# Performance work log

Measured on AMD Instinct MI355X. Metric: run time of the kernel, lower is better.

The kernel has to match this reference:

```python
import jax, jax.numpy as jnp
import numpy as np

EMBED_DIM = 1024


def setup_inputs() -> dict:
    key = jax.random.key(0)
    ks = jax.random.split(key, 8)
    B, S, D = 4, 2048, EMBED_DIM
    scale = 1.0 / np.sqrt(D)
    x = jax.random.normal(ks[0], (B, S, D), dtype=jnp.float32)
    mask = jnp.zeros((S, S), dtype=jnp.float32)
    # nn.Linear default init ~ U(-1/sqrt(fan_in), 1/sqrt(fan_in)); exact dist irrelevant for correctness
    w_q = jax.random.uniform(ks[1], (D, D), jnp.float32, -scale, scale)
    b_q = jax.random.uniform(ks[2], (D,), jnp.float32, -scale, scale)
    w_k = jax.random.uniform(ks[3], (D, D), jnp.float32, -scale, scale)
    b_k = jax.random.uniform(ks[4], (D,), jnp.float32, -scale, scale)
    w_v = jax.random.uniform(ks[5], (D, D), jnp.float32, -scale, scale)
    b_v = jax.random.uniform(ks[6], (D,), jnp.float32, -scale, scale)
    return {"x": x, "mask": mask, "w_q": w_q, "b_q": b_q,
            "w_k": w_k, "b_k": b_k, "w_v": w_v, "b_v": b_v}


def reference(x, mask, w_q, b_q, w_k, b_k, w_v, b_v):
    D = x.shape[-1]
    # nn.Linear computes x @ W^T + b
    Q = jnp.einsum('bsd,ed->bse', x, w_q) + b_q
    K = jnp.einsum('bsd,ed->bse', x, w_k) + b_k
    V = jnp.einsum('bsd,ed->bse', x, w_v) + b_v
    scores = jnp.einsum('bqd,bkd->bqk', Q, K) / jnp.sqrt(jnp.asarray(D, x.dtype))
    scores = scores + mask  # additive mask, broadcast over batch
    attn = jax.nn.softmax(scores, axis=-1)
    return jnp.einsum('bqk,bkd->bqd', attn, V)
```

## Files before the change

kernel.cpp:

```cpp
#include <hip/hip_runtime.h>


typedef __attribute__((ext_vector_type(8))) short short8;
typedef __attribute__((ext_vector_type(4))) short short4v;
typedef __attribute__((ext_vector_type(4))) float float4v;

__device__ __forceinline__ short f2bf(float f) {
  unsigned u = __builtin_bit_cast(unsigned, f);
  u += 0x7fffu + ((u >> 16) & 1u);
  return (short)(u >> 16);
}
__device__ __forceinline__ float bf2f(short s) {
  unsigned u = ((unsigned)(unsigned short)s) << 16;
  return __builtin_bit_cast(float, u);
}

__device__ __forceinline__ void gl2lds16(const void* g, void* l) {
  __builtin_amdgcn_global_load_lds((const __attribute__((address_space(1))) void*)g,
                                   (__attribute__((address_space(3))) void*)l, 16, 0, 0);
}

__global__ __launch_bounds__(256) void prep_kernel(const float* __restrict__ x,
                                                   const float* __restrict__ wq,
                                                   const float* __restrict__ wk,
                                                   const float* __restrict__ wv,
                                                   const float* __restrict__ bq,
                                                   const float* __restrict__ bk,
                                                   short* __restrict__ x_bf,
                                                   short* __restrict__ w_bf,
                                                   float* __restrict__ bcat) {
  int b = blockIdx.x;
  if (b < 3072) {
    int seg = b >> 10;
    const float* w = seg == 0 ? wq : (seg == 1 ? wk : wv);
    int i = (b - (seg << 10)) * 256 + threadIdx.x;
    float4v v = ((const float4v*)w)[i];
    short4v o;
    o.x = f2bf(v.x); o.y = f2bf(v.y); o.z = f2bf(v.z); o.w = f2bf(v.w);
    ((short4v*)(w_bf + (long)seg * 1048576))[i] = o;
  } else if (b < 11264) {
    int i = (b - 3072) * 256 + threadIdx.x;
    float4v v = ((const float4v*)x)[i];
    short4v o;
    o.x = f2bf(v.x); o.y = f2bf(v.y); o.z = f2bf(v.z); o.w = f2bf(v.w);
    ((short4v*)x_bf)[i] = o;
  } else {
    int i = (b - 11264) * 256 + threadIdx.x;
    if (i < 2048) bcat[i] = i < 1024 ? bq[i] : bk[i - 1024];
  }
}

__device__ __forceinline__ void stage_half(const short* __restrict__ g, int ld,
                                           int grow0, int kt, short* lds, int t) {
  const int r = t >> 3;
  const int cch = (t & 7) ^ (r & 7);
  const long co = (long)kt + cch * 8;
  gl2lds16(g + (long)(grow0 + r) * ld + co, lds + t * 8);
  gl2lds16(g + (long)(grow0 + 64 + r) * ld + co, lds + 4096 + t * 8);
}

template <int EPI, int MH>
__device__ __forceinline__ void gemm_body(const short* __restrict__ A,
                                          const short* __restrict__ Bm,
                                          void* __restrict__ C,
                                          const float* __restrict__ aux,
                                          float* __restrict__ rsum, float scale,
                                          int N, int Kd, int Bld, int m0, int n0,
                                          short (*As)[64], short (*Bs)[64]) {
  const int t = threadIdx.x;
  const int lane = t & 63;
  const int wave = t >> 6;
  const int wm = (wave >> 2) * 64 * MH;
  const int wn = (wave & 3) * 64;
  const int col = lane & 15, quad = lane >> 4;
  const int sw = col & 7;
  const int NT = Kd >> 6;
  constexpr int AS = 128 * MH;

  float4v acc[4 * MH][4] = {};

  stage_half(A, Kd, m0, 0, &As[0][0], t);
  if constexpr (MH == 2) stage_half(A, Kd, m0 + 128, 0, &As[128][0], t);
  stage_half(Bm, Bld, n0, 0, &Bs[0][0], t);
  stage_half(Bm, Bld, n0 + 128, 0, &Bs[128][0], t);
  if (NT > 1) {
    stage_half(A, Kd, m0, 64, &As[AS][0], t);
    if constexpr (MH == 2) stage_half(A, Kd, m0 + 128, 64, &As[AS + 128][0], t);
    stage_half(Bm, Bld, n0, 64, &Bs[256][0], t);
    stage_half(Bm, Bld, n0 + 128, 64, &Bs[384][0], t);
    if constexpr (MH == 2)
      asm volatile("s_waitcnt vmcnt(8)" ::: "memory");
    else
      asm volatile("s_waitcnt vmcnt(6)" ::: "memory");
  } else {
    asm volatile("s_waitcnt vmcnt(0)" ::: "memory");
  }
  __builtin_amdgcn_s_barrier();

  int ar = 0;
  int aw = 2 * AS;
  int br = 0;

  for (int k = 0; k < NT; ++k) {
    short8 a[4][2], b0[2][2], b1[2][2];

    if constexpr (MH == 2) {
#pragma unroll
      for (int i = 0; i < 4; ++i)
#pragma unroll
        for (int s = 0; s < 2; ++s)
          a[i][s] = *(const short8*)&As[ar + wm + i * 16 + col][(((s * 4 + quad) ^ sw)) * 8];
#pragma unroll
      for (int j = 0; j < 2; ++j)
#pragma unroll
        for (int s = 0; s < 2; ++s)
          b0[j][s] = *(const short8*)&Bs[br + wn + j * 16 + col][(((s * 4 + quad) ^ sw)) * 8];
      if (k + 2 < NT) stage_half(A, Kd, m0, (k + 2) * 64, &As[aw][0], t);
      __builtin_amdgcn_s_barrier();
      __builtin_amdgcn_s_setprio(1);
#pragma unroll
      for (int i = 0; i < 4; ++i)
#pragma unroll
        for (int j = 0; j < 2; ++j)
#pragma unroll
          for (int s = 0; s < 2; ++s)
            acc[i][j] = __builtin_amdgcn_mfma_f32_16x16x32_bf16(a[i][s], b0[j][s], acc[i][j], 0, 0, 0);
      __builtin_amdgcn_s_setprio(0);

#pragma unroll
      for (int j = 0; j < 2; ++j)
#pragma unroll
        for (int s = 0; s < 2; ++s)
          b1[j][s] = *(const short8*)&Bs[br + wn + (j + 2) * 16 + col][(((s * 4 + quad) ^ sw)) * 8];
      if (k + 2 < NT) stage_half(A, Kd, m0 + 128, (k + 2) * 64, &As[aw + 128][0], t);
      __builtin_amdgcn_s_barrier();
      __builtin_amdgcn_s_setprio(1);
#pragma unroll
      for (int i = 0; i < 4; ++i)
#pragma unroll
        for (int j = 0; j < 2; ++j)
#pragma unroll
          for (int s = 0; s < 2; ++s)
            acc[i][j + 2] = __builtin_amdgcn_mfma_f32_16x16x32_bf16(a[i][s], b1[j][s], acc[i][j + 2], 0, 0, 0);
      __builtin_amdgcn_s_setprio(0);

#pragma unroll
      for (int i = 0; i < 4; ++i)
#pragma unroll
        for (int s = 0; s < 2; ++s)
          a[i][s] = *(const short8*)&As[ar + wm + (i + 4) * 16 + col][(((s * 4 + quad) ^ sw)) * 8];
      if (k + 2 < NT) stage_half(Bm, Bld, n0, (k + 2) * 64, &Bs[br][0], t);
      __builtin_amdgcn_s_barrier();
      __builtin_amdgcn_s_setprio(1);
#pragma unroll
      for (int i = 0; i < 4; ++i)
#pragma unroll
        for (int j = 0; j < 2; ++j)
#pragma unroll
          for (int s = 0; s < 2; ++s)
            acc[i + 4][j + 2] = __builtin_amdgcn_mfma_f32_16x16x32_bf16(a[i][s], b1[j][s], acc[i + 4][j + 2], 0, 0, 0);
      __builtin_amdgcn_s_setprio(0);

      if (k + 2 < NT) stage_half(Bm, Bld, n0 + 128, (k + 2) * 64, &Bs[br + 128][0], t);
      if (k + 2 < NT) {
        asm volatile("s_waitcnt vmcnt(8)" ::: "memory");
      } else if (k + 1 < NT) {
        asm volatile("s_waitcnt vmcnt(0)" ::: "memory");
      }
      __builtin_amdgcn_s_barrier();
      __builtin_amdgcn_s_setprio(1);
#pragma unroll
      for (int i = 0; i < 4; ++i)
#pragma unroll
        for (int j = 0; j < 2; ++j)
#pragma unroll
          for (int s = 0; s < 2; ++s)
            acc[i + 4][j] = __builtin_amdgcn_mfma_f32_16x16x32_bf16(a[i][s], b0[j][s], acc[i + 4][j], 0, 0, 0);
      __builtin_amdgcn_s_setprio(0);
    } else {
#pragma unroll
      for (int i = 0; i < 4; ++i)
#pragma unroll
        for (int s = 0; s < 2; ++s)
          a[i][s] = *(const short8*)&As[ar + wm + i * 16 + col][(((s * 4 + quad) ^ sw)) * 8];
#pragma unroll
      for (int j = 0; j < 2; ++j)
#pragma unroll
        for (int s = 0; s < 2; ++s)
          b0[j][s] = *(const short8*)&Bs[br + wn + j * 16 + col][(((s * 4 + quad) ^ sw)) * 8];
      if (k + 2 < NT) stage_half(A, Kd, m0, (k + 2) * 64, &As[aw][0], t);
      __builtin_amdgcn_s_barrier();
      __builtin_amdgcn_s_setprio(1);
#pragma unroll
      for (int i = 0; i < 4; ++i)
#pragma unroll
        for (int j = 0; j < 2; ++j)
#pragma unroll
          for (int s = 0; s < 2; ++s)
            acc[i][j] = __builtin_amdgcn_mfma_f32_16x16x32_bf16(a[i][s], b0[j][s], acc[i][j], 0, 0, 0);
      __builtin_amdgcn_s_setprio(0);

#pragma unroll
      for (int j = 0; j < 2; ++j)
#pragma unroll
        for (int s = 0; s < 2; ++s)
          b1[j][s] = *(const short8*)&Bs[br + wn + (j + 2) * 16 + col][(((s * 4 + quad) ^ sw)) * 8];
      if (k + 2 < NT) {
        stage_half(Bm, Bld, n0, (k + 2) * 64, &Bs[br][0], t);
        stage_half(Bm, Bld, n0 + 128, (k + 2) * 64, &Bs[br + 128][0], t);
        asm volatile("s_waitcnt vmcnt(6)" ::: "memory");
      } else if (k + 1 < NT) {
        asm volatile("s_waitcnt vmcnt(0)" ::: "memory");
      }
      __builtin_amdgcn_s_barrier();
      __builtin_amdgcn_s_setprio(1);
#pragma unroll
      for (int i = 0; i < 4; ++i)
#pragma unroll
        for (int j = 0; j < 2; ++j)
#pragma unroll
          for (int s = 0; s < 2; ++s)
            acc[i][j + 2] = __builtin_amdgcn_mfma_f32_16x16x32_bf16(a[i][s], b1[j][s], acc[i][j + 2], 0, 0, 0);
      __builtin_amdgcn_s_setprio(0);
    }

    ar = (ar == 2 * AS) ? 0 : ar + AS;
    aw = (aw == 2 * AS) ? 0 : aw + AS;
    br ^= 256;
  }

  float* invb = (float*)&Bs[0][0];
  if (EPI == 2) {
    __syncthreads();
    if (t < 128 * MH) {
      float s = 0.f;
#pragma unroll
      for (int p = 0; p < 32; ++p) s += aux[p * 8192 + m0 + t];
      invb[t] = __builtin_amdgcn_rcpf(s);
    }
    __syncthreads();
  }

  const float LOG2E = 1.44269504f;
  const float c1 = scale * LOG2E;
#pragma unroll
  for (int i = 0; i < 4 * MH; ++i) {
    float invv[4], addm[4], rsum4[4] = {0.f, 0.f, 0.f, 0.f};
    if (EPI == 2) {
#pragma unroll
      for (int r = 0; r < 4; ++r) invv[r] = invb[wm + i * 16 + quad * 4 + r];
    }
    if (EPI == 3) {
#pragma unroll
      for (int r = 0; r < 4; ++r) addm[r] = aux[m0 + wm + i * 16 + quad * 4 + r];
    }
#pragma unroll
    for (int j = 0; j < 4; ++j) {
      const int n = n0 + wn + j * 16 + col;
      float addn = 0.f;
      if (EPI == 0) addn = aux[n];
#pragma unroll
      for (int r = 0; r < 4; ++r) {
        const int m = m0 + wm + i * 16 + quad * 4 + r;
        float v = acc[i][j][r];
        if (EPI == 0) {
          ((short*)C)[(long)m * N + n] = f2bf(v + addn);
        } else if (EPI == 1) {
          float mv = aux[(long)m * N + n];
          float e = exp2f(fmaf(v, c1, mv * LOG2E));
          short q = f2bf(e);
          ((short*)C)[(long)m * N + n] = q;
          rsum4[r] += bf2f(q);
        } else if (EPI == 2) {
          ((float*)C)[(long)m * N + n] = v * invv[r];
        } else {
          ((short*)C)[(long)m * N + n] = f2bf(v + addm[r]);
        }
      }
    }
    if (EPI == 1) {
#pragma unroll
      for (int r = 0; r < 4; ++r) {
        float s = rsum4[r];
        s += __shfl_xor(s, 1);
        s += __shfl_xor(s, 2);
        s += __shfl_xor(s, 4);
        s += __shfl_xor(s, 8);
        if (col == 0)
          rsum[(wave & 3) * 8192 + m0 + wm + i * 16 + quad * 4 + r] = s;
      }
    }
  }
}

__global__ __launch_bounds__(512, 2) void qkv_kernel(const short* __restrict__ x_bf,
                                                     const short* __restrict__ w_bf,
                                                     short* __restrict__ QK,
                                                     short* __restrict__ Vt,
                                                     const float* __restrict__ bcat,
                                                     const float* __restrict__ bv) {
  __shared__ alignas(16) short As[768][64];
  __shared__ alignas(16) short Bs[512][64];
  const int b = blockIdx.x;
  const int g = (b & 7) * 48 + (b >> 3);
  if (g < 256) {
    const int pair = g >> 1, bz = g & 1;
    const int m0 = (pair >> 2) * 256, n0 = (pair & 3) * 256;
    gemm_body<0, 2>(x_bf, w_bf + (long)bz * 1048576, QK + (long)bz * 8388608,
                    bcat + bz * 1024, nullptr, 1.f, 1024, 1024, 1024, m0, n0, As, Bs);
  } else {
    const int v = g - 256;
    const int m0 = (v >> 5) * 256, n0 = (v & 31) * 256;
    gemm_body<3, 2>(w_bf + 2097152, x_bf, Vt, bv, nullptr, 1.f,
                    8192, 1024, 1024, m0, n0, As, Bs);
  }
}

__global__ __launch_bounds__(512, 2) void scores_kernel(const short* __restrict__ Q,
                                                        const short* __restrict__ Kb,
                                                        short* __restrict__ P,
                                                        const float* __restrict__ mask,
                                                        float* __restrict__ rspart) {
  __shared__ alignas(16) short As[768][64];
  __shared__ alignas(16) short Bs[512][64];
  const int b = blockIdx.x;
  const int g = (b & 7) * 32 + (b >> 3);
  const int bz = g >> 6, t2 = g & 63;
  const int m0 = (t2 >> 3) * 256, n0 = (t2 & 7) * 256;
  gemm_body<1, 2>(Q + (long)bz * 2097152, Kb + (long)bz * 2097152,
                  P + (long)bz * 4194304, mask,
                  rspart + (long)(n0 >> 8) * 4 * 8192 + bz * 2048, 0.03125f,
                  2048, 1024, 1024, m0, n0, As, Bs);
}

__global__ __launch_bounds__(512, 2) void pv_kernel(const short* __restrict__ P,
                                                    const short* __restrict__ Vt,
                                                    float* __restrict__ out,
                                                    const float* __restrict__ rspart) {
  __shared__ alignas(16) short As[384][64];
  __shared__ alignas(16) short Bs[512][64];
  const int b = blockIdx.x;
  const int g = (b & 7) * 32 + (b >> 3);
  const int bz = g >> 6, t2 = g & 63;
  const int m0 = (t2 >> 2) * 128, n0 = (t2 & 3) * 256;
  gemm_body<2, 1>(P + (long)bz * 4194304, Vt + (long)bz * 2048,
                  out + (long)bz * 2097152, rspart + bz * 2048, nullptr, 1.f,
                  1024, 2048, 8192, m0, n0, As, Bs);
}

extern "C" void kernel_launch(void* const* d_in, const int* in_sizes, int n_in,
                              void* d_out, int out_size, void* d_ws, size_t ws_size,
                              hipStream_t stream) {
  const float* x    = (const float*)d_in[0];
  const float* mask = (const float*)d_in[1];
  const float* wq   = (const float*)d_in[2];
  const float* bq   = (const float*)d_in[3];
  const float* wk   = (const float*)d_in[4];
  const float* bk   = (const float*)d_in[5];
  const float* wv   = (const float*)d_in[6];
  const float* bv   = (const float*)d_in[7];
  float* out = (float*)d_out;

  char* ws = (char*)d_ws;
  const size_t MB = 1024 * 1024;
  short* x_bf   = (short*)(ws);
  float* rspart = (float*)(ws);
  short* w_bf   = (short*)(ws + 16 * MB);
  short* QK     = (short*)(ws + 22 * MB);
  short* Vt     = (short*)(ws + 54 * MB);
  short* P      = (short*)(ws + 70 * MB);
  float* bcat   = (float*)(ws + 70 * MB);

  prep_kernel<<<11272, 256, 0, stream>>>(x, wq, wk, wv, bq, bk, x_bf, w_bf, bcat);

  qkv_kernel<<<384, 512, 0, stream>>>(x_bf, w_bf, QK, Vt, bcat, bv);

  short* Q  = QK;
  short* Kb = QK + 8388608;

  scores_kernel<<<256, 512, 0, stream>>>(Q, Kb, P, mask, rspart);

  pv_kernel<<<256, 512, 0, stream>>>(P, Vt, out, rspart);
}
```

Before: 255.4 us.

## Fuse prep, QKV, scores and PV into one cooperative persistent kernel

```diff
diff --git a/kernel.cpp b/kernel.cpp
--- a/kernel.cpp
+++ b/kernel.cpp
@@ -1,4 +1,7 @@
 #include <hip/hip_runtime.h>
+#include <hip/hip_cooperative_groups.h>
+
+namespace cg = cooperative_groups;
 
 
 typedef __attribute__((ext_vector_type(8))) short short8;
@@ -18,6 +21,335 @@
 __device__ __forceinline__ void gl2lds16(const void* g, void* l) {
   __builtin_amdgcn_global_load_lds((const __attribute__((address_space(1))) void*)g,
                                    (__attribute__((address_space(3))) void*)l, 16, 0, 0);
+}
+
+__device__ unsigned g_vt_ctr;
+
+__device__ __forceinline__ void stage_half(const short* __restrict__ g, int ld,
+                                           int grow0, int kt, short* lds, int t) {
+  const int r = t >> 3;
+  const int cch = (t & 7) ^ (r & 7);
+  const long co = (long)kt + cch * 8;
+  gl2lds16(g + (long)(grow0 + r) * ld + co, lds + t * 8);
+  gl2lds16(g + (long)(grow0 + 64 + r) * ld + co, lds + 4096 + t * 8);
+}
+
+template <int EPI, int MH>
+__device__ __forceinline__ void gemm_body(const short* __restrict__ A,
+                                          const short* __restrict__ Bm,
+                                          void* __restrict__ C,
+                                          const float* __restrict__ aux,
+                                          float* __restrict__ rsum, float scale,
+                                          int N, int Kd, int Bld, int m0, int n0,
+                                          short (*As)[64], short (*Bs)[64]) {
+  const int t = threadIdx.x;
+  const int lane = t & 63;
+  const int wave = t >> 6;
+  const int wm = (wave >> 2) * 64 * MH;
+  const int wn = (wave & 3) * 64;
+  const int col = lane & 15, quad = lane >> 4;
+  const int sw = col & 7;
+  const int NT = Kd >> 6;
+  constexpr int AS = 128 * MH;
+
+  float4v acc[4 * MH][4] = {};
+
+  stage_half(A, Kd, m0, 0, &As[0][0], t);
+  if constexpr (MH == 2) stage_half(A, Kd, m0 + 128, 0, &As[128][0], t);
+  stage_half(Bm, Bld, n0, 0, &Bs[0][0], t);
+  stage_half(Bm, Bld, n0 + 128, 0, &Bs[128][0], t);
+  if (NT > 1) {
+    stage_half(A, Kd, m0, 64, &As[AS][0], t);
+    if constexpr (MH == 2) stage_half(A, Kd, m0 + 128, 64, &As[AS + 128][0], t);
+    stage_half(Bm, Bld, n0, 64, &Bs[256][0], t);
+    stage_half(Bm, Bld, n0 + 128, 64, &Bs[384][0], t);
+    if constexpr (MH == 2)
+      asm volatile("s_waitcnt vmcnt(8)" ::: "memory");
+    else
+      asm volatile("s_waitcnt vmcnt(6)" ::: "memory");
+  } else {
+    asm volatile("s_waitcnt vmcnt(0)" ::: "memory");
+  }
+  __builtin_amdgcn_s_barrier();
+
+  int ar = 0;
+  int aw = 2 * AS;
+  int br = 0;
+
+  for (int k = 0; k < NT; ++k) {
+    short8 a[4][2], b0[2][2], b1[2][2];
+
+    if constexpr (MH == 2) {
+#pragma unroll
+      for (int i = 0; i < 4; ++i)
+#pragma unroll
+        for (int s = 0; s < 2; ++s)
+          a[i][s] = *(const short8*)&As[ar + wm + i * 16 + col][(((s * 4 + quad) ^ sw)) * 8];
+#pragma unroll
+      for (int j = 0; j < 2; ++j)
+#pragma unroll
+        for (int s = 0; s < 2; ++s)
+          b0[j][s] = *(const short8*)&Bs[br + wn + j * 16 + col][(((s * 4 + quad) ^ sw)) * 8];
+      if (k + 2 < NT) stage_half(A, Kd, m0, (k + 2) * 64, &As[aw][0], t);
+      __builtin_amdgcn_s_barrier();
+      __builtin_amdgcn_s_setprio(1);
+#pragma unroll
+      for (int i = 0; i < 4; ++i)
+#pragma unroll
+        for (int j = 0; j < 2; ++j)
+#pragma unroll
+          for (int s = 0; s < 2; ++s)
+            acc[i][j] = __builtin_amdgcn_mfma_f32_16x16x32_bf16(a[i][s], b0[j][s], acc[i][j], 0, 0, 0);
+      __builtin_amdgcn_s_setprio(0);
+
+#pragma unroll
+      for (int j = 0; j < 2; ++j)
+#pragma unroll
+        for (int s = 0; s < 2; ++s)
+          b1[j][s] = *(const short8*)&Bs[br + wn + (j + 2) * 16 + col][(((s * 4 + quad) ^ sw)) * 8];
+      if (k + 2 < NT) stage_half(A, Kd, m0 + 128, (k + 2) * 64, &As[aw + 128][0], t);
+      __builtin_amdgcn_s_barrier();
+      __builtin_amdgcn_s_setprio(1);
+#pragma unroll
+      for (int i = 0; i < 4; ++i)
+#pragma unroll
+        for (int j = 0; j < 2; ++j)
+#pragma unroll
+          for (int s = 0; s < 2; ++s)
+            acc[i][j + 2] = __builtin_amdgcn_mfma_f32_16x16x32_bf16(a[i][s], b1[j][s], acc[i][j + 2], 0, 0, 0);
+      __builtin_amdgcn_s_setprio(0);
+
+#pragma unroll
+      for (int i = 0; i < 4; ++i)
+#pragma unroll
+        for (int s = 0; s < 2; ++s)
+          a[i][s] = *(const short8*)&As[ar + wm + (i + 4) * 16 + col][(((s * 4 + quad) ^ sw)) * 8];
+      if (k + 2 < NT) stage_half(Bm, Bld, n0, (k + 2) * 64, &Bs[br][0], t);
+      __builtin_amdgcn_s_barrier();
+      __builtin_amdgcn_s_setprio(1);
+#pragma unroll
+      for (int i = 0; i < 4; ++i)
+#pragma unroll
+        for (int j = 0; j < 2; ++j)
+#pragma unroll
+          for (int s = 0; s < 2; ++s)
+            acc[i + 4][j + 2] = __builtin_amdgcn_mfma_f32_16x16x32_bf16(a[i][s], b1[j][s], acc[i + 4][j + 2], 0, 0, 0);
+      __builtin_amdgcn_s_setprio(0);
+
+      if (k + 2 < NT) stage_half(Bm, Bld, n0 + 128, (k + 2) * 64, &Bs[br + 128][0], t);
+      if (k + 2 < NT) {
+        asm volatile("s_waitcnt vmcnt(8)" ::: "memory");
+      } else if (k + 1 < NT) {
+        asm volatile("s_waitcnt vmcnt(0)" ::: "memory");
+      }
+      __builtin_amdgcn_s_barrier();
+      __builtin_amdgcn_s_setprio(1);
+#pragma unroll
+      for (int i = 0; i < 4; ++i)
+#pragma unroll
+        for (int j = 0; j < 2; ++j)
+#pragma unroll
+          for (int s = 0; s < 2; ++s)
+            acc[i + 4][j] = __builtin_amdgcn_mfma_f32_16x16x32_bf16(a[i][s], b0[j][s], acc[i + 4][j], 0, 0, 0);
+      __builtin_amdgcn_s_setprio(0);
+    } else {
+#pragma unroll
+      for (int i = 0; i < 4; ++i)
+#pragma unroll
+        for (int s = 0; s < 2; ++s)
+          a[i][s] = *(const short8*)&As[ar + wm + i * 16 + col][(((s * 4 + quad) ^ sw)) * 8];
+#pragma unroll
+      for (int j = 0; j < 2; ++j)
+#pragma unroll
+        for (int s = 0; s < 2; ++s)
+          b0[j][s] = *(const short8*)&Bs[br + wn + j * 16 + col][(((s * 4 + quad) ^ sw)) * 8];
+      if (k + 2 < NT) stage_half(A, Kd, m0, (k + 2) * 64, &As[aw][0], t);
+      __builtin_amdgcn_s_barrier();
+      __builtin_amdgcn_s_setprio(1);
+#pragma unroll
+      for (int i = 0; i < 4; ++i)
+#pragma unroll
+        for (int j = 0; j < 2; ++j)
+#pragma unroll
+          for (int s = 0; s < 2; ++s)
+            acc[i][j] = __builtin_amdgcn_mfma_f32_16x16x32_bf16(a[i][s], b0[j][s], acc[i][j], 0, 0, 0);
+      __builtin_amdgcn_s_setprio(0);
+
+#pragma unroll
+      for (int j = 0; j < 2; ++j)
+#pragma unroll
+        for (int s = 0; s < 2; ++s)
+          b1[j][s] = *(const short8*)&Bs[br + wn + (j + 2) * 16 + col][(((s * 4 + quad) ^ sw)) * 8];
+      if (k + 2 < NT) {
+        stage_half(Bm, Bld, n0, (k + 2) * 64, &Bs[br][0], t);
+        stage_half(Bm, Bld, n0 + 128, (k + 2) * 64, &Bs[br + 128][0], t);
+        asm volatile("s_waitcnt vmcnt(6)" ::: "memory");
+      } else if (k + 1 < NT) {
+        asm volatile("s_waitcnt vmcnt(0)" ::: "memory");
+      }
+      __builtin_amdgcn_s_barrier();
+      __builtin_amdgcn_s_setprio(1);
+#pragma unroll
+      for (int i = 0; i < 4; ++i)
+#pragma unroll
+        for (int j = 0; j < 2; ++j)
+#pragma unroll
+          for (int s = 0; s < 2; ++s)
+            acc[i][j + 2] = __builtin_amdgcn_mfma_f32_16x16x32_bf16(a[i][s], b1[j][s], acc[i][j + 2], 0, 0, 0);
+      __builtin_amdgcn_s_setprio(0);
+    }
+
+    ar = (ar == 2 * AS) ? 0 : ar + AS;
+    aw = (aw == 2 * AS) ? 0 : aw + AS;
+    br ^= 256;
+  }
+
+  float* invb = (float*)&Bs[0][0];
+  if (EPI == 2) {
+    __syncthreads();
+    if (t < 128 * MH) {
+      float s = 0.f;
+#pragma unroll
+      for (int p = 0; p < 32; ++p) s += aux[p * 8192 + m0 + t];
+      invb[t] = __builtin_amdgcn_rcpf(s);
+    }
+    __syncthreads();
+  }
+
+  const float LOG2E = 1.44269504f;
+  const float c1 = scale * LOG2E;
+#pragma unroll
+  for (int i = 0; i < 4 * MH; ++i) {
+    float invv[4], addm[4], rsum4[4] = {0.f, 0.f, 0.f, 0.f};
+    if (EPI == 2) {
+#pragma unroll
+      for (int r = 0; r < 4; ++r) invv[r] = invb[wm + i * 16 + quad * 4 + r];
+    }
+    if (EPI == 3) {
+#pragma unroll
+      for (int r = 0; r < 4; ++r) addm[r] = aux[m0 + wm + i * 16 + quad * 4 + r];
+    }
+#pragma unroll
+    for (int j = 0; j < 4; ++j) {
+      const int n = n0 + wn + j * 16 + col;
+      float addn = 0.f;
+      if (EPI == 0) addn = aux[n];
+#pragma unroll
+      for (int r = 0; r < 4; ++r) {
+        const int m = m0 + wm + i * 16 + quad * 4 + r;
+        float v = acc[i][j][r];
+        if (EPI == 0) {
+          ((short*)C)[(long)m * N + n] = f2bf(v + addn);
+        } else if (EPI == 1) {
+          float mv = aux[(long)m * N + n];
+          float e = exp2f(fmaf(v, c1, mv * LOG2E));
+          short q = f2bf(e);
+          ((short*)C)[(long)m * N + n] = q;
+          rsum4[r] += bf2f(q);
+        } else if (EPI == 2) {
+          ((float*)C)[(long)m * N + n] = v * invv[r];
+        } else {
+          ((short*)C)[(long)m * N + n] = f2bf(v + addm[r]);
+        }
+      }
+    }
+    if (EPI == 1) {
+#pragma unroll
+      for (int r = 0; r < 4; ++r) {
+        float s = rsum4[r];
+        s += __shfl_xor(s, 1);
+        s += __shfl_xor(s, 2);
+        s += __shfl_xor(s, 4);
+        s += __shfl_xor(s, 8);
+        if (col == 0)
+          rsum[(wave & 3) * 8192 + m0 + wm + i * 16 + quad * 4 + r] = s;
+      }
+    }
+  }
+}
+
+__global__ __launch_bounds__(512, 2) void fused_kernel(
+    const float* __restrict__ x, const float* __restrict__ mask,
+    const float* __restrict__ wq, const float* __restrict__ bq,
+    const float* __restrict__ wk, const float* __restrict__ bk,
+    const float* __restrict__ wv, const float* __restrict__ bv,
+    float* __restrict__ out, char* ws) {
+  __shared__ alignas(16) short As[768][64];
+  __shared__ alignas(16) short Bs[512][64];
+  const size_t MB = 1048576;
+  short* x_bf   = (short*)ws;
+  float* rspart = (float*)ws;
+  short* w_bf   = (short*)(ws + 16 * MB);
+  short* QK     = (short*)(ws + 22 * MB);
+  short* Vt     = (short*)(ws + 54 * MB);
+  short* P      = (short*)(ws + 70 * MB);
+  float* bcat   = (float*)(ws + 70 * MB);
+
+  const int bid = blockIdx.x;
+  const int tid = threadIdx.x;
+  const unsigned gtid = (unsigned)bid * 512u + (unsigned)tid;
+
+  if (gtid == 0) g_vt_ctr = 0u;
+#pragma unroll 1
+  for (unsigned i = gtid; i < 786432u; i += 131072u) {
+    const unsigned seg = i >> 18, idx = i & 262143u;
+    const float* w = seg == 0 ? wq : (seg == 1 ? wk : wv);
+    float4v v = ((const float4v*)w)[idx];
+    short4v o;
+    o.x = f2bf(v.x); o.y = f2bf(v.y); o.z = f2bf(v.z); o.w = f2bf(v.w);
+    ((short4v*)(w_bf + (long)seg * 1048576))[idx] = o;
+  }
+#pragma unroll 1
+  for (unsigned i = gtid; i < 2097152u; i += 131072u) {
+    float4v v = ((const float4v*)x)[i];
+    short4v o;
+    o.x = f2bf(v.x); o.y = f2bf(v.y); o.z = f2bf(v.z); o.w = f2bf(v.w);
+    ((short4v*)x_bf)[i] = o;
+  }
+  if (gtid < 2048u) bcat[gtid] = gtid < 1024u ? bq[gtid] : bk[gtid - 1024u];
+  __threadfence();
+  cg::this_grid().sync();
+
+  const int g = (bid & 7) * 32 + (bid >> 3);
+
+  {
+    const int pair = g >> 1, bz = g & 1;
+    const int m0 = (pair >> 2) * 256, n0 = (pair & 3) * 256;
+    gemm_body<0, 2>(x_bf, w_bf + (long)bz * 1048576, QK + (long)bz * 8388608,
+                    bcat + bz * 1024, nullptr, 1.f, 1024, 1024, 1024, m0, n0, As, Bs);
+  }
+  unsigned* vt_sh = (unsigned*)&As[0][0];
+  for (;;) {
+    if (tid == 0) *vt_sh = atomicAdd(&g_vt_ctr, 1u);
+    __syncthreads();
+    const unsigned v = *vt_sh;
+    __syncthreads();
+    if (v >= 128u) break;
+    const int m0 = (int)(v >> 5) * 256, n0 = (int)(v & 31u) * 256;
+    gemm_body<3, 2>(w_bf + 2097152, x_bf, Vt, bv, nullptr, 1.f,
+                    8192, 1024, 1024, m0, n0, As, Bs);
+  }
+  __threadfence();
+  cg::this_grid().sync();
+
+  {
+    const int bz = g >> 6, t2 = g & 63;
+    const int m0 = (t2 >> 3) * 256, n0 = (t2 & 7) * 256;
+    gemm_body<1, 2>(QK + (long)bz * 2097152, QK + 8388608 + (long)bz * 2097152,
+                    P + (long)bz * 4194304, mask,
+                    rspart + (long)(n0 >> 8) * 4 * 8192 + bz * 2048, 0.03125f,
+                    2048, 1024, 1024, m0, n0, As, Bs);
+  }
+  __threadfence();
+  cg::this_grid().sync();
+
+  {
+    const int bz = g >> 6, t2 = g & 63;
+    const int m0 = (t2 >> 2) * 128, n0 = (t2 & 3) * 256;
+    gemm_body<2, 1>(P + (long)bz * 4194304, Vt + (long)bz * 2048,
+                    out + (long)bz * 2097152, rspart + bz * 2048, nullptr, 1.f,
+                    1024, 2048, 8192, m0, n0, As, Bs);
+  }
 }
 
 __global__ __launch_bounds__(256) void prep_kernel(const float* __restrict__ x,
@@ -50,249 +382,6 @@
   }
 }
 
-__device__ __forceinline__ void stage_half(const short* __restrict__ g, int ld,
-                                           int grow0, int kt, short* lds, int t) {
-  const int r = t >> 3;
-  const int cch = (t & 7) ^ (r & 7);
-  const long co = (long)kt + cch * 8;
-  gl2lds16(g + (long)(grow0 + r) * ld + co, lds + t * 8);
-  gl2lds16(g + (long)(grow0 + 64 + r) * ld + co, lds + 4096 + t * 8);
-}
-
-template <int EPI, int MH>
-__device__ __forceinline__ void gemm_body(const short* __restrict__ A,
-                                          const short* __restrict__ Bm,
-                                          void* __restrict__ C,
-                                          const float* __restrict__ aux,
-                                          float* __restrict__ rsum, float scale,
-                                          int N, int Kd, int Bld, int m0, int n0,
-                                          short (*As)[64], short (*Bs)[64]) {
-  const int t = threadIdx.x;
-  const int lane = t & 63;
-  const int wave = t >> 6;
-  const int wm = (wave >> 2) * 64 * MH;
-  const int wn = (wave & 3) * 64;
-  const int col = lane & 15, quad = lane >> 4;
-  const int sw = col & 7;
-  const int NT = Kd >> 6;
-  constexpr int AS = 128 * MH;
-
-  float4v acc[4 * MH][4] = {};
-
-  stage_half(A, Kd, m0, 0, &As[0][0], t);
-  if constexpr (MH == 2) stage_half(A, Kd, m0 + 128, 0, &As[128][0], t);
-  stage_half(Bm, Bld, n0, 0, &Bs[0][0], t);
-  stage_half(Bm, Bld, n0 + 128, 0, &Bs[128][0], t);
-  if (NT > 1) {
-    stage_half(A, Kd, m0, 64, &As[AS][0], t);
-    if constexpr (MH == 2) stage_half(A, Kd, m0 + 128, 64, &As[AS + 128][0], t);
-    stage_half(Bm, Bld, n0, 64, &Bs[256][0], t);
-    stage_half(Bm, Bld, n0 + 128, 64, &Bs[384][0], t);
-    if constexpr (MH == 2)
-      asm volatile("s_waitcnt vmcnt(8)" ::: "memory");
-    else
-      asm volatile("s_waitcnt vmcnt(6)" ::: "memory");
-  } else {
-    asm volatile("s_waitcnt vmcnt(0)" ::: "memory");
-  }
-  __builtin_amdgcn_s_barrier();
-
-  int ar = 0;
-  int aw = 2 * AS;
-  int br = 0;
-
-  for (int k = 0; k < NT; ++k) {
-    short8 a[4][2], b0[2][2], b1[2][2];
-
-    if constexpr (MH == 2) {
-#pragma unroll
-      for (int i = 0; i < 4; ++i)
-#pragma unroll
-        for (int s = 0; s < 2; ++s)
-          a[i][s] = *(const short8*)&As[ar + wm + i * 16 + col][(((s * 4 + quad) ^ sw)) * 8];
-#pragma unroll
-      for (int j = 0; j < 2; ++j)
-#pragma unroll
-        for (int s = 0; s < 2; ++s)
-          b0[j][s] = *(const short8*)&Bs[br + wn + j * 16 + col][(((s * 4 + quad) ^ sw)) * 8];
-      if (k + 2 < NT) stage_half(A, Kd, m0, (k + 2) * 64, &As[aw][0], t);
-      __builtin_amdgcn_s_barrier();
-      __builtin_amdgcn_s_setprio(1);
-#pragma unroll
-      for (int i = 0; i < 4; ++i)
-#pragma unroll
-        for (int j = 0; j < 2; ++j)
-#pragma unroll
-          for (int s = 0; s < 2; ++s)
-            acc[i][j] = __builtin_amdgcn_mfma_f32_16x16x32_bf16(a[i][s], b0[j][s], acc[i][j], 0, 0, 0);
-      __builtin_amdgcn_s_setprio(0);
-
-#pragma unroll
-      for (int j = 0; j < 2; ++j)
-#pragma unroll
-        for (int s = 0; s < 2; ++s)
-          b1[j][s] = *(const short8*)&Bs[br + wn + (j + 2) * 16 + col][(((s * 4 + quad) ^ sw)) * 8];
-      if (k + 2 < NT) stage_half(A, Kd, m0 + 128, (k + 2) * 64, &As[aw + 128][0], t);
-      __builtin_amdgcn_s_barrier();
-      __builtin_amdgcn_s_setprio(1);
-#pragma unroll
-      for (int i = 0; i < 4; ++i)
-#pragma unroll
-        for (int j = 0; j < 2; ++j)
-#pragma unroll
-          for (int s = 0; s < 2; ++s)
-            acc[i][j + 2] = __builtin_amdgcn_mfma_f32_16x16x32_bf16(a[i][s], b1[j][s], acc[i][j + 2], 0, 0, 0);
-      __builtin_amdgcn_s_setprio(0);
-
-#pragma unroll
-      for (int i = 0; i < 4; ++i)
-#pragma unroll
-        for (int s = 0; s < 2; ++s)
-          a[i][s] = *(const short8*)&As[ar + wm + (i + 4) * 16 + col][(((s * 4 + quad) ^ sw)) * 8];
-      if (k + 2 < NT) stage_half(Bm, Bld, n0, (k + 2) * 64, &Bs[br][0], t);
-      __builtin_amdgcn_s_barrier();
-      __builtin_amdgcn_s_setprio(1);
-#pragma unroll
-      for (int i = 0; i < 4; ++i)
-#pragma unroll
-        for (int j = 0; j < 2; ++j)
-#pragma unroll
-          for (int s = 0; s < 2; ++s)
-            acc[i + 4][j + 2] = __builtin_amdgcn_mfma_f32_16x16x32_bf16(a[i][s], b1[j][s], acc[i + 4][j + 2], 0, 0, 0);
-      __builtin_amdgcn_s_setprio(0);
-
-      if (k + 2 < NT) stage_half(Bm, Bld, n0 + 128, (k + 2) * 64, &Bs[br + 128][0], t);
-      if (k + 2 < NT) {
-        asm volatile("s_waitcnt vmcnt(8)" ::: "memory");
-      } else if (k + 1 < NT) {
-        asm volatile("s_waitcnt vmcnt(0)" ::: "memory");
-      }
-      __builtin_amdgcn_s_barrier();
-      __builtin_amdgcn_s_setprio(1);
-#pragma unroll
-      for (int i = 0; i < 4; ++i)
-#pragma unroll
-        for (int j = 0; j < 2; ++j)
-#pragma unroll
-          for (int s = 0; s < 2; ++s)
-            acc[i + 4][j] = __builtin_amdgcn_mfma_f32_16x16x32_bf16(a[i][s], b0[j][s], acc[i + 4][j], 0, 0, 0);
-      __builtin_amdgcn_s_setprio(0);
-    } else {
-#pragma unroll
-      for (int i = 0; i < 4; ++i)
-#pragma unroll
-        for (int s = 0; s < 2; ++s)
-          a[i][s] = *(const short8*)&As[ar + wm + i * 16 + col][(((s * 4 + quad) ^ sw)) * 8];
-#pragma unroll
-      for (int j = 0; j < 2; ++j)
-#pragma unroll
-        for (int s = 0; s < 2; ++s)
-          b0[j][s] = *(const short8*)&Bs[br + wn + j * 16 + col][(((s * 4 + quad) ^ sw)) * 8];
-      if (k + 2 < NT) stage_half(A, Kd, m0, (k + 2) * 64, &As[aw][0], t);
-      __builtin_amdgcn_s_barrier();
-      __builtin_amdgcn_s_setprio(1);
-#pragma unroll
-      for (int i = 0; i < 4; ++i)
-#pragma unroll
-        for (int j = 0; j < 2; ++j)
-#pragma unroll
-          for (int s = 0; s < 2; ++s)
-            acc[i][j] = __builtin_amdgcn_mfma_f32_16x16x32_bf16(a[i][s], b0[j][s], acc[i][j], 0, 0, 0);
-      __builtin_amdgcn_s_setprio(0);
-
-#pragma unroll
-      for (int j = 0; j < 2; ++j)
-#pragma unroll
-        for (int s = 0; s < 2; ++s)
-          b1[j][s] = *(const short8*)&Bs[br + wn + (j + 2) * 16 + col][(((s * 4 + quad) ^ sw)) * 8];
-      if (k + 2 < NT) {
-        stage_half(Bm, Bld, n0, (k + 2) * 64, &Bs[br][0], t);
-        stage_half(Bm, Bld, n0 + 128, (k + 2) * 64, &Bs[br + 128][0], t);
-        asm volatile("s_waitcnt vmcnt(6)" ::: "memory");
-      } else if (k + 1 < NT) {
-        asm volatile("s_waitcnt vmcnt(0)" ::: "memory");
-      }
-      __builtin_amdgcn_s_barrier();
-      __builtin_amdgcn_s_setprio(1);
-#pragma unroll
-      for (int i = 0; i < 4; ++i)
-#pragma unroll
-        for (int j = 0; j < 2; ++j)
-#pragma unroll
-          for (int s = 0; s < 2; ++s)
-            acc[i][j + 2] = __builtin_amdgcn_mfma_f32_16x16x32_bf16(a[i][s], b1[j][s], acc[i][j + 2], 0, 0, 0);
-      __builtin_amdgcn_s_setprio(0);
-    }
-
-    ar = (ar == 2 * AS) ? 0 : ar + AS;
-    aw = (aw == 2 * AS) ? 0 : aw + AS;
-    br ^= 256;
-  }
-
-  float* invb = (float*)&Bs[0][0];
-  if (EPI == 2) {
-    __syncthreads();
-    if (t < 128 * MH) {
-      float s = 0.f;
-#pragma unroll
-      for (int p = 0; p < 32; ++p) s += aux[p * 8192 + m0 + t];
-      invb[t] = __builtin_amdgcn_rcpf(s);
-    }
-    __syncthreads();
-  }
-
-  const float LOG2E = 1.44269504f;
-  const float c1 = scale * LOG2E;
-#pragma unroll
-  for (int i = 0; i < 4 * MH; ++i) {
-    float invv[4], addm[4], rsum4[4] = {0.f, 0.f, 0.f, 0.f};
-    if (EPI == 2) {
-#pragma unroll
-      for (int r = 0; r < 4; ++r) invv[r] = invb[wm + i * 16 + quad * 4 + r];
-    }
-    if (EPI == 3) {
-#pragma unroll
-      for (int r = 0; r < 4; ++r) addm[r] = aux[m0 + wm + i * 16 + quad * 4 + r];
-    }
-#pragma unroll
-    for (int j = 0; j < 4; ++j) {
-      const int n = n0 + wn + j * 16 + col;
-      float addn = 0.f;
-      if (EPI == 0) addn = aux[n];
-#pragma unroll
-      for (int r = 0; r < 4; ++r) {
-        const int m = m0 + wm + i * 16 + quad * 4 + r;
-        float v = acc[i][j][r];
-        if (EPI == 0) {
-          ((short*)C)[(long)m * N + n] = f2bf(v + addn);
-        } else if (EPI == 1) {
-          float mv = aux[(long)m * N + n];
-          float e = exp2f(fmaf(v, c1, mv * LOG2E));
-          short q = f2bf(e);
-          ((short*)C)[(long)m * N + n] = q;
-          rsum4[r] += bf2f(q);
-        } else if (EPI == 2) {
-          ((float*)C)[(long)m * N + n] = v * invv[r];
-        } else {
-          ((short*)C)[(long)m * N + n] = f2bf(v + addm[r]);
-        }
-      }
-    }
-    if (EPI == 1) {
-#pragma unroll
-      for (int r = 0; r < 4; ++r) {
-        float s = rsum4[r];
-        s += __shfl_xor(s, 1);
-        s += __shfl_xor(s, 2);
-        s += __shfl_xor(s, 4);
-        s += __shfl_xor(s, 8);
-        if (col == 0)
-          rsum[(wave & 3) * 8192 + m0 + wm + i * 16 + quad * 4 + r] = s;
-      }
-    }
-  }
-}
-
 __global__ __launch_bounds__(512, 2) void qkv_kernel(const short* __restrict__ x_bf,
                                                      const short* __restrict__ w_bf,
                                                      short* __restrict__ QK,
@@ -360,25 +449,26 @@
   const float* wv   = (const float*)d_in[6];
   const float* bv   = (const float*)d_in[7];
   float* out = (float*)d_out;
-
   char* ws = (char*)d_ws;
-  const size_t MB = 1024 * 1024;
-  short* x_bf   = (short*)(ws);
-  float* rspart = (float*)(ws);
-  short* w_bf   = (short*)(ws + 16 * MB);
-  short* QK     = (short*)(ws + 22 * MB);
-  short* Vt     = (short*)(ws + 54 * MB);
-  short* P      = (short*)(ws + 70 * MB);
-  float* bcat   = (float*)(ws + 70 * MB);
-
-  prep_kernel<<<11272, 256, 0, stream>>>(x, wq, wk, wv, bq, bk, x_bf, w_bf, bcat);
-
-  qkv_kernel<<<384, 512, 0, stream>>>(x_bf, w_bf, QK, Vt, bcat, bv);
-
-  short* Q  = QK;
-  short* Kb = QK + 8388608;
-
-  scores_kernel<<<256, 512, 0, stream>>>(Q, Kb, P, mask, rspart);
-
-  pv_kernel<<<256, 512, 0, stream>>>(P, Vt, out, rspart);
-}
+
+  void* kargs[] = {(void*)&x, (void*)&mask, (void*)&wq, (void*)&bq, (void*)&wk,
+                   (void*)&bk, (void*)&wv, (void*)&bv, (void*)&out, (void*)&ws};
+  hipError_t err = hipLaunchCooperativeKernel((void*)fused_kernel, dim3(256),
+                                              dim3(512), kargs, 0, stream);
+  if (err != hipSuccess) {
+    const size_t MB = 1024 * 1024;
+    short* x_bf   = (short*)(ws);
+    float* rspart = (float*)(ws);
+    short* w_bf   = (short*)(ws + 16 * MB);
+    short* QK     = (short*)(ws + 22 * MB);
+    short* Vt     = (short*)(ws + 54 * MB);
+    short* P      = (short*)(ws + 70 * MB);
+    float* bcat   = (float*)(ws + 70 * MB);
+    prep_kernel<<<11272, 256, 0, stream>>>(x, wq, wk, wv, bq, bk, x_bf, w_bf, bcat);
+    qkv_kernel<<<384, 512, 0, stream>>>(x_bf, w_bf, QK, Vt, bcat, bv);
+    short* Q  = QK;
+    short* Kb = QK + 8388608;
+    scores_kernel<<<256, 512, 0, stream>>>(Q, Kb, P, mask, rspart);
+    pv_kernel<<<256, 512, 0, stream>>>(P, Vt, out, rspart);
+  }
+}
```

Measured after the change: 543.3 us. 2.13x slower.
